# Kernel optimization log

Measured on AMD Instinct MI355X. Metric: run time of the kernel, lower is better.

The kernel has to match this reference:

```python
import jax, jax.numpy as jnp
import numpy as np

BN_EPS = 1e-5

def conv1x1(x, w, b):
    # x: [N,C,T,V], w: [O,C], b: [O]
    return jnp.einsum('nctv,oc->notv', x, w) + b[None, :, None, None]

def conv9(x, w, b):
    # (9,1) temporal conv, padding (4,0). x: [N,C,T,V], w: [O,C,9], b: [O]
    out = jax.lax.conv_general_dilated(
        x, w[:, :, :, None], window_strides=(1, 1), padding=((4, 4), (0, 0)),
        dimension_numbers=('NCHW', 'OIHW', 'NCHW'))
    return out + b[None, :, None, None]

def attn_adj(f1, f2):
    # f1,f2: [N,inter,T,V] -> softmax over rows (axis -2) of [N,V,V]
    N, ic, T, V = f1.shape
    a1 = jnp.transpose(f1, (0, 3, 1, 2)).reshape(N, V, ic * T)  # permute(0,3,1,2).view
    a2 = f2.reshape(N, ic * T, V)
    scores = jnp.einsum('nvk,nkw->nvw', a1, a2) / (ic * T)
    return jax.nn.softmax(scores, axis=-2)


def setup_inputs() -> dict:
    key = jax.random.key(0)
    ks = jax.random.split(key, 16)
    N, C, T, V, S, IC = 16, 256, 64, 25, 3, 64
    s = lambda k, shape, sc=0.05: jax.random.normal(k, shape, dtype=jnp.float32) * sc
    return {
        'x': jax.random.normal(ks[0], (N, C, T, V), dtype=jnp.float32),
        'A': jax.random.uniform(ks[1], (S, V, V), dtype=jnp.float32),
        'PA': s(ks[2], (S, V, V), 1e-3),
        'wa': s(ks[3], (S, IC, C)), 'ba': jnp.zeros((S, IC), jnp.float32),
        'wb': s(ks[4], (S, IC, C)), 'bb': jnp.zeros((S, IC), jnp.float32),
        'wT1': s(ks[5], (S, IC, C, 9)), 'bT1': jnp.zeros((S, IC), jnp.float32),
        'wT2': s(ks[6], (S, IC, C, 9)), 'bT2': jnp.zeros((S, IC), jnp.float32),
        'wST11': s(ks[7], (S, IC, C, 9)), 'bST11': jnp.zeros((S, IC), jnp.float32),
        'wST12': s(ks[8], (S, IC, C, 9)), 'bST12': jnp.zeros((S, IC), jnp.float32),
        'wd': s(ks[9], (S, C, C)), 'bd': jnp.zeros((S, C), jnp.float32),
        'gamma': jnp.ones((C,), jnp.float32), 'beta': jnp.zeros((C,), jnp.float32),
        'bn_mean': jnp.zeros((C,), jnp.float32), 'bn_var': jnp.ones((C,), jnp.float32),
    }


def reference(x, A, PA, wa, ba, wb, bb, wT1, bT1, wT2, bT2,
              wST11, bST11, wST12, bST12, wd, bd, gamma, beta, bn_mean, bn_var):
    N, C, T, V = x.shape
    I = jnp.eye(V, dtype=x.dtype)
    # Chebyshev-like static graph transforms (computed once in __init__ in torch)
    A_ch4s = jax.nn.softmax((8 * A**4 - 4 * A**2 - 4 * A + I) / V, axis=-2)
    A_ch3 = 4 * A**2 - A - 2 * I
    A_all = A_ch3 + A_ch4s + PA  # [3,V,V]

    xf = x.reshape(N, C * T, V)
    y = 0.0
    for i in range(3):
        A1 = attn_adj(conv1x1(x, wa[i], ba[i]), conv1x1(x, wb[i], bb[i]))
        AT = attn_adj(conv9(x, wT1[i], bT1[i]), conv9(x, wT2[i], bT2[i]))
        # ModuleList append quirk: even i -> 1x1 conv (center tap), odd i -> (9,1) conv
        if i % 2 == 0:
            s1 = conv1x1(x, wST11[i, :, :, 4], bST11[i])
            s2 = conv1x1(x, wST12[i, :, :, 4], bST12[i])
        else:
            s1 = conv9(x, wST11[i], bST11[i])
            s2 = conv9(x, wST12[i], bST12[i])
        AST = attn_adj(s1, s2)
        Ai = A_all[i] + A1 + AT + AST  # [N,V,V]
        z = jnp.einsum('nkv,nvw->nkw', xf, Ai).reshape(N, C, T, V)
        y = y + conv1x1(z, wd[i], bd[i])

    yb = (y - bn_mean[None, :, None, None]) * (gamma[None, :, None, None]
         / jnp.sqrt(bn_var[None, :, None, None] + BN_EPS)) + beta[None, :, None, None]
    return jax.nn.relu(yb + x)  # down is identity (in_channels == out_channels)
```

## Files before the change

kernel.cpp:

```cpp
#include <hip/hip_runtime.h>
#include <hip/hip_bf16.h>

#define NN 16
#define CC 256
#define TT 64
#define VV 25
#define ICC 64
#define TV 1600
#define CTV 409600
#define NICTV 1638400

typedef __bf16 v8bf __attribute__((ext_vector_type(8)));
typedef __bf16 v4bf __attribute__((ext_vector_type(4)));
typedef float f32x16 __attribute__((ext_vector_type(16)));

struct ConvPairs {
  const __bf16* wA[5];
  const __bf16* wB[5];
  const float*  bA[5];
  const float*  bB[5];
};

__device__ __forceinline__ void gl_lds16(const __bf16* g, __bf16* l){
  __builtin_amdgcn_global_load_lds(
      (const __attribute__((address_space(1))) unsigned int*)g,
      (__attribute__((address_space(3))) unsigned int*)l, 16, 0, 0);
}

__global__ __launch_bounds__(256) void prep_k(
    const float* __restrict__ x, __bf16* __restrict__ xt,
    const float* __restrict__ wT1, const float* __restrict__ wT2,
    const float* __restrict__ wST11, const float* __restrict__ wST12,
    __bf16* __restrict__ wT1p, __bf16* __restrict__ wT2p,
    __bf16* __restrict__ wS1p, __bf16* __restrict__ wS2p,
    const float* __restrict__ wa, const float* __restrict__ wb,
    __bf16* __restrict__ wabp, __bf16* __restrict__ wScp,
    const float* __restrict__ wd, __bf16* __restrict__ wdb,
    const float* __restrict__ A, const float* __restrict__ PA,
    float* __restrict__ Aall, __bf16* __restrict__ zp){
  __shared__ __align__(16) float smf[64*65];
  __bf16* smb = (__bf16*)smf;
  int b = blockIdx.x;
  int tid = threadIdx.x;
  if (b < 64){
    int t = b >> 3, ch64 = (b >> 1) & 3, o2 = b & 1;
    const float* src; __bf16* dst;
    if (t < 3)      { src = wT1  + (size_t)t*147456;     dst = wT1p + (size_t)t*147456; }
    else if (t < 6) { src = wT2  + (size_t)(t-3)*147456; dst = wT2p + (size_t)(t-3)*147456; }
    else if (t == 6){ src = wST11 + 147456;              dst = wS1p; }
    else            { src = wST12 + 147456;              dst = wS2p; }
    const float* in = src + (size_t)(o2*32)*2304 + ch64*576;
    for (int i = tid; i < 32*576; i += 256){
      int row = i / 576, cc = i % 576;
      smb[i] = (__bf16)in[(size_t)row*2304 + cc];
    }
    __syncthreads();
    for (int i = tid; i < 18432; i += 256){
      int e = i & 7, l = (i >> 3) & 63, ks = (i >> 9) & 1;
      int r10 = i >> 10;
      int tap = r10 % 9, chh = r10 / 9;
      int ol = l & 31, hh = l >> 5;
      int cl = ks*16 + hh*8 + e;
      int c64 = chh*32 + cl;
      int ch8 = ch64*2 + chh;
      dst[(size_t)((((ch8*9 + tap)*2 + ks)*2 + o2)*512) + l*8 + e]
          = smb[ol*576 + c64*9 + tap];
    }
  } else if (b < 74){
    int u = b - 64;
    for (int it = 0; it < 8; ++it){
      int i = tid + it*256;
      int e = i & 7, l = (i >> 3) & 63, o2 = (i >> 9) & 1;
      int ks = (i >> 10) & 1, ch = i >> 11;
      int ol = l & 31, hh = l >> 5;
      int o = o2*32 + ol;
      int c = ch*32 + ks*16 + hh*8 + e;
      __bf16 v;
      if (u < 6){
        const float* w = (u < 3) ? (wa + (size_t)u*16384) : (wb + (size_t)(u-3)*16384);
        v = (__bf16)w[(size_t)o*256 + c];
      } else {
        int i9 = ((u == 6) || (u == 8)) ? 0 : 2;
        const float* w = ((u < 8) ? wST11 : wST12) + (size_t)i9*147456;
        v = (__bf16)w[((size_t)o*256 + c)*9 + 4];
      }
      __bf16* dst = (u < 6) ? (wabp + (size_t)u*16384) : (wScp + (size_t)(u-6)*16384);
      dst[i] = v;
    }
  } else if (b < 842){
    int i = (b-74)*256 + tid;
    if (i < 196608) wdb[i] = (__bf16)wd[i];
  } else if (b == 842){
    int t = tid;
    if (t < 75){
      int s = t / 25, w = t % 25;
      float a[25], m[25];
      float mx = -3.4e38f;
      for (int v = 0; v < 25; ++v){
        float av = A[(s*25 + v)*25 + w];
        a[v] = av;
        float d = (v == w) ? 1.f : 0.f;
        float mm = (8.f*av*av*av*av - 4.f*av*av - 4.f*av + d) * 0.04f;
        m[v] = mm;
        mx = fmaxf(mx, mm);
      }
      float sum = 0.f;
      for (int v = 0; v < 25; ++v){ float e = __expf(m[v]-mx); m[v] = e; sum += e; }
      float inv = 1.f/sum;
      for (int v = 0; v < 25; ++v){
        float av = a[v];
        float d = (v == w) ? 1.f : 0.f;
        Aall[(s*25+v)*25 + w] = m[v]*inv + 4.f*av*av - av - 2.f*d + PA[(s*25+v)*25+w];
      }
    } else if (t >= 128){
      zp[t-128] = (__bf16)0.f;
    }
  } else {
    int idx = b - 843;
    int p0 = (idx % 25)*64, c0 = ((idx/25) & 3)*64, n = idx/100;
    for (int i = tid; i < 4096; i += 256){
      int cc = i >> 6, pp = i & 63;
      smf[cc*65+pp] = x[(size_t)n*CTV + (size_t)(c0+cc)*TV + p0 + pp];
    }
    __syncthreads();
    for (int i = tid; i < 4096; i += 256){
      int pp = i >> 6, cc = i & 63;
      xt[((size_t)n*TV + p0+pp)*256 + c0+cc] = (__bf16)smf[cc*65+pp];
    }
  }
}

template<int NTAPS, int MINW>
__global__ __launch_bounds__(512, MINW) void conv15_k(const __bf16* __restrict__ xt,
    ConvPairs cp, const __bf16* __restrict__ zp, __bf16* __restrict__ fbuf){
  extern __shared__ __bf16 sm[];
  constexpr int HALO  = (NTAPS==9) ? 100 : 0;
  constexpr int NROWS = 256 + 2*HALO;
  constexpr int SLOTS = NROWS*4;
  constexpr int KSTG  = (SLOTS + 511)/512;
  constexpr int NSTEP = NTAPS*2;
  constexpr int AELE  = NTAPS*2*2*512;
  constexpr int ASLT  = 2*AELE/8;
  constexpr int DEP   = (NSTEP >= 3) ? 3 : 2;
  int p0 = blockIdx.x*256;
  int n  = blockIdx.y;
  int pr = blockIdx.z;
  int tid = threadIdx.x;
  int lane = tid & 63;
  int wave = tid >> 6;
  int which = wave >> 2, wq = wave & 3;
  int h = lane >> 5, l31 = lane & 31;
  const __bf16* xtn = xt + (size_t)n*CTV;
  const __bf16* wg0 = cp.wA[pr];
  const __bf16* wg1 = cp.wB[pr];
  __bf16* xb0 = sm;
  __bf16* xb1 = sm + NROWS*32;
  __bf16* Ab  = sm + 2*NROWS*32;

  f32x16 acc[2][2];
  #pragma unroll
  for (int a=0;a<2;++a)
    #pragma unroll
    for (int b=0;b<2;++b)
      #pragma unroll
      for (int r=0;r<16;++r) acc[a][b][r] = 0.f;

  int rowbase = wq*64 + l31;

  auto stageX = [&](__bf16* bn, int ch){
    #pragma unroll
    for (int k=0; k<KSTG; ++k){
      int slot = k*512 + tid;
      if ((SLOTS & 511) && slot >= SLOTS) continue;
      const __bf16* src;
      if (NTAPS == 1){
        int l31s = slot & 31, f = slot >> 5;
        int h_ = f & 1, ks_ = (f >> 1) & 1, pblk = f >> 2;
        int pg = p0 + pblk*32 + l31s;
        src = (pg < 1600) ? (xtn + (size_t)pg*256 + ch*32 + ks_*16 + h_*8)
                          : zp;
      } else {
        int row = slot >> 2, g2 = slot & 3;
        int g = (g2 - (row>>1)) & 3;
        int pg = p0 - HALO + row;
        src = ((unsigned)pg < 1600u) ? (xtn + (size_t)pg*256 + ch*32 + g*8)
                                     : zp;
      }
      gl_lds16(src, bn + (size_t)slot*8);
    }
  };
  auto stageA = [&](int ch){
    #pragma unroll
    for (int k=0; k<(ASLT+511)/512; ++k){
      int slot = k*512 + tid;
      if ((ASLT & 511) && slot >= ASLT) continue;
      int cv = (slot >= AELE/8) ? 1 : 0;
      int off = (slot - cv*(AELE/8))*8;
      const __bf16* src = (cv ? wg1 : wg0) + (size_t)ch*AELE + off;
      gl_lds16(src, Ab + cv*AELE + off);
    }
  };
  const __bf16* aw = Ab + which*AELE + lane*8;
  auto ldA = [&](int s, v8bf* aa){
    int off = s*1024;
    aa[0] = *(const v8bf*)(aw + off);
    aa[1] = *(const v8bf*)(aw + off + 512);
  };
  auto ldB = [&](const __bf16* bc, int s, v8bf* bb){
    int tap = s >> 1, ks = s & 1;
    #pragma unroll
    for (int pq=0; pq<2; ++pq){
      if (NTAPS == 1){
        int frag = ((wq*2 + pq)*2 + ks)*2 + h;
        bb[pq] = *(const v8bf*)(bc + frag*256 + l31*8);
      } else {
        int row = tap*25 + rowbase + pq*32;
        int gs = ((ks*2 + h) + (row>>1)) & 3;
        bb[pq] = *(const v8bf*)(bc + row*32 + gs*8);
      }
    }
  };

  stageA(0);
  stageX(xb0, 0);
  __syncthreads();

  v8bf ar[DEP][2], bR[DEP][2];
  for (int ch=0; ch<8; ++ch){
    const __bf16* bc = (ch & 1) ? xb1 : xb0;
    __bf16*       bn = (ch & 1) ? xb0 : xb1;
    if (ch < 7) stageX(bn, ch+1);
    #pragma unroll
    for (int i=0; i<DEP; ++i){
      if (i < NSTEP){ ldA(i, ar[i]); ldB(bc, i, bR[i]); }
    }
    #pragma unroll
    for (int s=0; s<NSTEP; ++s){
      int c = s % DEP;
      v8bf A0 = ar[c][0], A1 = ar[c][1];
      v8bf B0 = bR[c][0], B1 = bR[c][1];
      if (s+DEP < NSTEP){
        ldB(bc, s+DEP, bR[c]);
        ldA(s+DEP, ar[c]);
      }
      __builtin_amdgcn_s_setprio(1);
      acc[0][0] = __builtin_amdgcn_mfma_f32_32x32x16_bf16(A0, B0, acc[0][0], 0,0,0);
      acc[1][0] = __builtin_amdgcn_mfma_f32_32x32x16_bf16(A1, B0, acc[1][0], 0,0,0);
      acc[0][1] = __builtin_amdgcn_mfma_f32_32x32x16_bf16(A0, B1, acc[0][1], 0,0,0);
      acc[1][1] = __builtin_amdgcn_mfma_f32_32x32x16_bf16(A1, B1, acc[1][1], 0,0,0);
      __builtin_amdgcn_s_setprio(0);
    }
    __syncthreads();
    if (ch < 7) stageA(ch+1);
    __syncthreads();
  }

  const float* bias = which ? cp.bB[pr] : cp.bA[pr];
  __bf16* outb = fbuf + (size_t)(pr*2 + which)*NICTV + (size_t)n*TV*64;
  #pragma unroll
  for (int pq=0; pq<2; ++pq){
    int p = p0 + wq*64 + pq*32 + l31;
    if (p >= 1600) continue;
    __bf16* orow = outb + (size_t)p*64;
    #pragma unroll
    for (int of=0; of<2; ++of){
      #pragma unroll
      for (int g=0; g<4; ++g){
        int og = of*32 + 8*g + 4*h;
        v4bf pk;
        #pragma unroll
        for (int j=0;j<4;++j) pk[j] = (__bf16)(acc[of][pq][4*g+j] + bias[og+j]);
        *(v4bf*)(orow + og) = pk;
      }
    }
  }
}

__global__ __launch_bounds__(256, 2) void ugemm6_k(const __bf16* __restrict__ xt,
    const __bf16* __restrict__ wdb, __bf16* __restrict__ ubuf){
  __shared__ __bf16 sm[64*256];
  int p0 = blockIdx.x*64;
  int n  = blockIdx.y;
  int tid = threadIdx.x;
  int lane = tid & 63;
  int os = tid >> 6;
  int h = lane >> 5, l31 = lane & 31;
  const __bf16* xtn = xt + (size_t)n*CTV;

  for (int s2 = tid; s2 < 64*32; s2 += 256){
    int row = s2 >> 5, g = s2 & 31;
    uint4 val = *(const uint4*)(xtn + (size_t)(p0+row)*256 + g*8);
    int gs = (g + row) & 31;
    *(uint4*)(sm + row*256 + gs*8) = val;
  }
  __syncthreads();

  auto ldB = [&](int ks, v8bf* bb){
    #pragma unroll
    for (int pq=0; pq<2; ++pq){
      int row = pq*32 + l31;
      int gs = ((ks*2 + h) + row) & 31;
      bb[pq] = *(const v8bf*)(sm + row*256 + gs*8);
    }
  };

  for (int br=0; br<3; ++br){
    const __bf16* wl = wdb + ((size_t)br*256 + os*64 + l31)*256 + h*8;
    auto ldA = [&](int ks, v8bf& A0, v8bf& A1){
      A0 = *(const v8bf*)(wl + ks*16);
      A1 = *(const v8bf*)(wl + (size_t)32*256 + ks*16);
    };
    f32x16 acc[2][2];
    #pragma unroll
    for (int a=0;a<2;++a)
      #pragma unroll
      for (int b=0;b<2;++b)
        #pragma unroll
        for (int r=0;r<16;++r) acc[a][b][r] = 0.f;

    v8bf a0[4], a1[4];
    ldA(0, a0[0], a1[0]);
    ldA(1, a0[1], a1[1]);
    ldA(2, a0[2], a1[2]);
    ldA(3, a0[3], a1[3]);
    v8bf bR[2][2];
    ldB(0, bR[0]);
    ldB(1, bR[1]);
    #pragma unroll
    for (int ks=0; ks<16; ++ks){
      int c2 = ks & 1, cur = ks & 3;
      v8bf B0 = bR[c2][0], B1 = bR[c2][1];
      v8bf A0 = a0[cur], A1 = a1[cur];
      if (ks+2 < 16) ldB(ks+2, bR[c2]);
      if (ks+4 < 16) ldA(ks+4, a0[cur], a1[cur]);
      acc[0][0] = __builtin_amdgcn_mfma_f32_32x32x16_bf16(A0, B0, acc[0][0], 0,0,0);
      acc[1][0] = __builtin_amdgcn_mfma_f32_32x32x16_bf16(A1, B0, acc[1][0], 0,0,0);
      acc[0][1] = __builtin_amdgcn_mfma_f32_32x32x16_bf16(A0, B1, acc[0][1], 0,0,0);
      acc[1][1] = __builtin_amdgcn_mfma_f32_32x32x16_bf16(A1, B1, acc[1][1], 0,0,0);
    }

    #pragma unroll
    for (int pq=0; pq<2; ++pq){
      int p = p0 + pq*32 + l31;
      __bf16* out = ubuf + ((size_t)(br*NN + n)*TV + p)*256;
      #pragma unroll
      for (int oq=0; oq<2; ++oq){
        #pragma unroll
        for (int g=0; g<4; ++g){
          int og = os*64 + oq*32 + 8*g + 4*h;
          v4bf pk;
          #pragma unroll
          for (int j=0;j<4;++j) pk[j] = (__bf16)acc[oq][pq][4*g+j];
          *(v4bf*)(out + og) = pk;
        }
      }
    }
  }
}

__global__ __launch_bounds__(256) void scores_m_k(const __bf16* __restrict__ fbuf,
                                                  float* __restrict__ part, int pairbase){
  int n = blockIdx.y, pr = blockIdx.z;
  int tid = threadIdx.x;
  int lane = tid & 63;
  int wave = tid >> 6;
  int chunk = blockIdx.x*4 + wave;
  int h = lane >> 5, l31 = lane & 31;
  const __bf16* f1 = fbuf + (size_t)(pr*2)*NICTV   + (size_t)n*TV*64;
  const __bf16* f2 = fbuf + (size_t)(pr*2+1)*NICTV + (size_t)n*TV*64;
  int t0 = chunk*4;

  f32x16 acc;
  #pragma unroll
  for (int r=0;r<16;++r) acc[r] = 0.f;

  auto off = [&](int s)->size_t{
    int t = t0 + (s>>2), og = s&3;
    return ((size_t)(t*25 + l31))*64 + og*16 + h*8;
  };
  v8bf A[4], B[4];
  #pragma unroll
  for (int i=0; i<4; ++i){
    size_t o = off(i);
    A[i] = *(const v8bf*)(f1+o); B[i] = *(const v8bf*)(f2+o);
  }
  #pragma unroll
  for (int s=0; s<16; ++s){
    int cur = s & 3;
    v8bf Ac = A[cur], Bc = B[cur];
    if (s+4 < 16){
      size_t o2 = off(s+4);
      A[cur] = *(const v8bf*)(f1+o2);
      B[cur] = *(const v8bf*)(f2+o2);
    }
    acc = __builtin_amdgcn_mfma_f32_32x32x16_bf16(Ac, Bc, acc, 0,0,0);
  }

  size_t tile = (((size_t)(pairbase+pr)*NN + n)*16 + chunk);
  float* pt = part + tile*1024;
  #pragma unroll
  for (int r=0; r<16; ++r){
    int row = (r&3) + 8*(r>>2) + 4*h;
    pt[row*32 + l31] = acc[r];
  }
}

__global__ __launch_bounds__(64) void reduce_all_k(const float* __restrict__ part,
    const float* __restrict__ Aall, float* __restrict__ Ai3){
  const int pairbr[9] = {0,1,2,0,2, 0,1,2,1};
  int n = blockIdx.x, w = blockIdx.y;
  int lane = threadIdx.x;
  float accbr[3] = {0.f, 0.f, 0.f};
  for (int pr=0; pr<9; ++pr){
    float s = 0.f;
    if (lane < 25){
      const float* pp = part + (((size_t)pr*NN + n)*16)*1024 + lane*32 + w;
      #pragma unroll
      for (int ch=0; ch<16; ++ch) s += pp[(size_t)ch*1024];
    }
    s *= (1.f/4096.f);
    float mval = (lane<25) ? s : -3.4e38f;
    #pragma unroll
    for (int d=32; d>0; d>>=1) mval = fmaxf(mval, __shfl_xor(mval, d));
    float e = (lane<25) ? __expf(s - mval) : 0.f;
    float sum = e;
    #pragma unroll
    for (int d=32; d>0; d>>=1) sum += __shfl_xor(sum, d);
    accbr[pairbr[pr]] += e / sum;
  }
  if (lane < 25){
    #pragma unroll
    for (int br=0; br<3; ++br)
      Ai3[((size_t)br*NN + n)*625 + lane*25 + w] =
        Aall[br*625 + lane*25 + w] + accbr[br];
  }
}

__global__ __launch_bounds__(256) void yep_k(const float* __restrict__ x,
    const float* __restrict__ Ai3, const __bf16* __restrict__ ubuf,
    const float* __restrict__ bd, const float* __restrict__ gamma,
    const float* __restrict__ beta, const float* __restrict__ bnm,
    const float* __restrict__ bnv, float* __restrict__ out){
  __shared__ float ais[3][25*28];
  int t = blockIdx.x, n = blockIdx.y, o = threadIdx.x;
  for (int l=o; l<2100; l+=256){
    int br = l/700, r = l%700;
    int v = r/28, w = r%28;
    ais[br][v*28+w] = (w<25) ? Ai3[((size_t)br*NN + n)*625 + v*25 + w] : 0.f;
  }
  __syncthreads();
  float y[28];
  #pragma unroll
  for (int w=0;w<28;++w) y[w]=0.f;
  for (int br=0; br<3; ++br){
    const __bf16* up = ubuf + ((size_t)(br*NN + n)*TV + t*25)*256 + o;
    float uv[25];
    #pragma unroll
    for (int v=0;v<25;++v) uv[v] = (float)up[(size_t)v*256];
    const float* ab = ais[br];
    for (int v=0; v<25; ++v){
      float u = uv[v];
      #pragma unroll
      for (int j=0; j<7; ++j){
        float4 a4 = *(const float4*)(ab + v*28 + 4*j);
        y[4*j+0] = fmaf(u, a4.x, y[4*j+0]);
        y[4*j+1] = fmaf(u, a4.y, y[4*j+1]);
        y[4*j+2] = fmaf(u, a4.z, y[4*j+2]);
        y[4*j+3] = fmaf(u, a4.w, y[4*j+3]);
      }
    }
  }
  float bsum = bd[o] + bd[256+o] + bd[512+o];
  float sc = gamma[o] * rsqrtf(bnv[o] + 1e-5f);
  float m  = bnm[o], be = beta[o];
  const float* xr = x + (size_t)n*CTV + (size_t)o*TV + t*25;
  float* orow = out + (size_t)n*CTV + (size_t)o*TV + t*25;
  #pragma unroll
  for (int w=0; w<25; ++w)
    orow[w] = fmaxf((y[w] + bsum - m)*sc + be + xr[w], 0.f);
}

extern "C" void kernel_launch(void* const* d_in, const int* in_sizes, int n_in,
                              void* d_out, int out_size, void* d_ws, size_t ws_size,
                              hipStream_t stream) {
  const float* x     = (const float*)d_in[0];
  const float* A     = (const float*)d_in[1];
  const float* PA    = (const float*)d_in[2];
  const float* wa    = (const float*)d_in[3];
  const float* ba    = (const float*)d_in[4];
  const float* wb    = (const float*)d_in[5];
  const float* bb    = (const float*)d_in[6];
  const float* wT1   = (const float*)d_in[7];
  const float* bT1   = (const float*)d_in[8];
  const float* wT2   = (const float*)d_in[9];
  const float* bT2   = (const float*)d_in[10];
  const float* wST11 = (const float*)d_in[11];
  const float* bST11 = (const float*)d_in[12];
  const float* wST12 = (const float*)d_in[13];
  const float* bST12 = (const float*)d_in[14];
  const float* wd    = (const float*)d_in[15];
  const float* bd    = (const float*)d_in[16];
  const float* gamma = (const float*)d_in[17];
  const float* beta  = (const float*)d_in[18];
  const float* bnm   = (const float*)d_in[19];
  const float* bnv   = (const float*)d_in[20];

  char* W = (char*)d_ws;
  float*  Aall = (float*)W;  W += 8192;
  __bf16* zp   = (__bf16*)W; W += 256;
  float*  Ai3  = (float*)W;  W += 122880;
  __bf16* wabp = (__bf16*)W; W += 196608;
  __bf16* wScp = (__bf16*)W; W += 131072;
  __bf16* wT1p = (__bf16*)W; W += 884736;
  __bf16* wT2p = (__bf16*)W; W += 884736;
  __bf16* wS1p = (__bf16*)W; W += 294912;
  __bf16* wS2p = (__bf16*)W; W += 294912;
  __bf16* wdb  = (__bf16*)W; W += 393216;
  __bf16* xt   = (__bf16*)W; W += 13107200;
  char* R = W;               W += 39321600;
  float*  part = (float*)W;  W += 9437184;
  __bf16* fbuf = (__bf16*)R;
  __bf16* ubuf = (__bf16*)R;

  prep_k<<<2443, 256, 0, stream>>>(x, xt, wT1, wT2, wST11, wST12,
                                   wT1p, wT2p, wS1p, wS2p,
                                   wa, wb, wabp, wScp, wd, wdb, A, PA, Aall, zp);

  {
    ConvPairs cp;
    for (int i=0;i<3;++i){
      cp.wA[i] = wabp + (size_t)i*16384;      cp.wB[i] = wabp + (size_t)(3+i)*16384;
      cp.bA[i] = ba + i*64;                   cp.bB[i] = bb + i*64;
    }
    int evens[2] = {0, 2};
    for (int j=0;j<2;++j){
      int i = evens[j];
      cp.wA[3+j] = wScp + (size_t)j*16384;    cp.wB[3+j] = wScp + (size_t)(2+j)*16384;
      cp.bA[3+j] = bST11 + i*64;              cp.bB[3+j] = bST12 + i*64;
    }
    conv15_k<1,4><<<dim3(7,16,5), 512, 40960, stream>>>(xt, cp, zp, fbuf);
    scores_m_k<<<dim3(4,16,5), 256, 0, stream>>>(fbuf, part, 0);
  }

  {
    ConvPairs cp;
    for (int i=0;i<3;++i){
      cp.wA[i] = wT1p + (size_t)i*147456;  cp.wB[i] = wT2p + (size_t)i*147456;
      cp.bA[i] = bT1 + i*64;               cp.bB[i] = bT2 + i*64;
    }
    cp.wA[3] = wS1p;  cp.wB[3] = wS2p;
    cp.bA[3] = bST11 + 64;  cp.bB[3] = bST12 + 64;
    cp.wA[4] = cp.wA[3]; cp.wB[4] = cp.wB[3]; cp.bA[4] = cp.bA[3]; cp.bB[4] = cp.bB[3];
    conv15_k<9,2><<<dim3(7,16,4), 512, 132096, stream>>>(xt, cp, zp, fbuf);
    scores_m_k<<<dim3(4,16,4), 256, 0, stream>>>(fbuf, part, 5);
  }

  ugemm6_k<<<dim3(25,16), 256, 0, stream>>>(xt, wdb, ubuf);
  reduce_all_k<<<dim3(16,25), 64, 0, stream>>>(part, Aall, Ai3);
  yep_k<<<dim3(64,16), 256, 0, stream>>>(x, Ai3, ubuf, bd, gamma, beta, bnm, bnv,
                                         (float*)d_out);
}
```

Before: 328.4 us.

## Pre-reduce score partials in LDS, restructure softmax finalize, coalesce epilogue via LDS

The scores kernel now sums its four waves' 32x32 partial tiles in shared memory before writing, so the partial buffer holds 4 tiles per (pair,n) instead of 16. The finalize kernel is regrouped per (n, branch) with one thread per column that computes the softmax serially over 25 rows, replacing the shuffle-based per-column launch. The yep epilogue stages x and out through shared memory so global reads and writes are contiguous across threads instead of strided by TV. The changes add syncs and shared-memory use, and the finalize kernel runs only 48 small blocks.

New measurement: 354.8 us. +8.0%, slower.

```diff
diff --git a/kernel.cpp b/kernel.cpp
--- a/kernel.cpp
+++ b/kernel.cpp
@@ -358,13 +358,14 @@
   }
 }
 
-__global__ __launch_bounds__(256) void scores_m_k(const __bf16* __restrict__ fbuf,
-                                                  float* __restrict__ part, int pairbase){
-  int n = blockIdx.y, pr = blockIdx.z;
+__global__ __launch_bounds__(256) void scores_m2_k(const __bf16* __restrict__ fbuf,
+                                                   float* __restrict__ part, int pairbase){
+  __shared__ float smp[4][1024];
+  int bx = blockIdx.x, n = blockIdx.y, pr = blockIdx.z;
   int tid = threadIdx.x;
   int lane = tid & 63;
   int wave = tid >> 6;
-  int chunk = blockIdx.x*4 + wave;
+  int chunk = bx*4 + wave;
   int h = lane >> 5, l31 = lane & 31;
   const __bf16* f1 = fbuf + (size_t)(pr*2)*NICTV   + (size_t)n*TV*64;
   const __bf16* f2 = fbuf + (size_t)(pr*2+1)*NICTV + (size_t)n*TV*64;
@@ -396,43 +397,53 @@
     acc = __builtin_amdgcn_mfma_f32_32x32x16_bf16(Ac, Bc, acc, 0,0,0);
   }
 
-  size_t tile = (((size_t)(pairbase+pr)*NN + n)*16 + chunk);
-  float* pt = part + tile*1024;
   #pragma unroll
   for (int r=0; r<16; ++r){
     int row = (r&3) + 8*(r>>2) + 4*h;
-    pt[row*32 + l31] = acc[r];
-  }
-}
-
-__global__ __launch_bounds__(64) void reduce_all_k(const float* __restrict__ part,
+    smp[wave][row*32 + l31] = acc[r];
+  }
+  __syncthreads();
+  for (int j = tid; j < 1024; j += 256){
+    float s = smp[0][j] + smp[1][j] + smp[2][j] + smp[3][j];
+    part[(((size_t)(pairbase+pr)*NN + n)*4 + bx)*1024 + j] = s;
+  }
+}
+
+__global__ __launch_bounds__(64) void finalize_k(const float* __restrict__ part,
     const float* __restrict__ Aall, float* __restrict__ Ai3){
-  const int pairbr[9] = {0,1,2,0,2, 0,1,2,1};
-  int n = blockIdx.x, w = blockIdx.y;
-  int lane = threadIdx.x;
-  float accbr[3] = {0.f, 0.f, 0.f};
-  for (int pr=0; pr<9; ++pr){
-    float s = 0.f;
-    if (lane < 25){
-      const float* pp = part + (((size_t)pr*NN + n)*16)*1024 + lane*32 + w;
-      #pragma unroll
-      for (int ch=0; ch<16; ++ch) s += pp[(size_t)ch*1024];
-    }
-    s *= (1.f/4096.f);
-    float mval = (lane<25) ? s : -3.4e38f;
-    #pragma unroll
-    for (int d=32; d>0; d>>=1) mval = fmaxf(mval, __shfl_xor(mval, d));
-    float e = (lane<25) ? __expf(s - mval) : 0.f;
-    float sum = e;
-    #pragma unroll
-    for (int d=32; d>0; d>>=1) sum += __shfl_xor(sum, d);
-    accbr[pairbr[pr]] += e / sum;
-  }
-  if (lane < 25){
-    #pragma unroll
-    for (int br=0; br<3; ++br)
-      Ai3[((size_t)br*NN + n)*625 + lane*25 + w] =
-        Aall[br*625 + lane*25 + w] + accbr[br];
+  int n = blockIdx.x, br = blockIdx.y;
+  int w = threadIdx.x;
+  const int prs0[3] = {0,3,5}, prs1[3] = {1,6,8}, prs2[3] = {2,4,7};
+  const int* prs = (br==0) ? prs0 : (br==1) ? prs1 : prs2;
+  float accv[25];
+  #pragma unroll
+  for (int v=0;v<25;++v) accv[v] = 0.f;
+  for (int k=0;k<3;++k){
+    int pr = prs[k];
+    const float* pb = part + ((size_t)pr*NN + n)*4096;
+    float sv[25];
+    float mx = -3.4e38f;
+    #pragma unroll
+    for (int v=0;v<25;++v){
+      float s = 0.f;
+      if (w < 25)
+        s = pb[v*32+w] + pb[1024+v*32+w] + pb[2048+v*32+w] + pb[3072+v*32+w];
+      s *= (1.f/4096.f);
+      sv[v] = s;
+      mx = fmaxf(mx, s);
+    }
+    float sum = 0.f;
+    #pragma unroll
+    for (int v=0;v<25;++v){ float e = __expf(sv[v]-mx); sv[v] = e; sum += e; }
+    float inv = 1.f/sum;
+    #pragma unroll
+    for (int v=0;v<25;++v) accv[v] += sv[v]*inv;
+  }
+  if (w < 25){
+    #pragma unroll
+    for (int v=0;v<25;++v)
+      Ai3[((size_t)br*NN + n)*625 + v*25 + w] =
+        Aall[br*625 + v*25 + w] + accv[v];
   }
 }
 
@@ -442,11 +453,16 @@
     const float* __restrict__ beta, const float* __restrict__ bnm,
     const float* __restrict__ bnv, float* __restrict__ out){
   __shared__ float ais[3][25*28];
+  __shared__ float xs[6400];
   int t = blockIdx.x, n = blockIdx.y, o = threadIdx.x;
   for (int l=o; l<2100; l+=256){
     int br = l/700, r = l%700;
     int v = r/28, w = r%28;
     ais[br][v*28+w] = (w<25) ? Ai3[((size_t)br*NN + n)*625 + v*25 + w] : 0.f;
+  }
+  for (int li=o; li<6400; li+=256){
+    int oo = li/25, ww = li%25;
+    xs[li] = x[(size_t)n*CTV + (size_t)oo*TV + t*25 + ww];
   }
   __syncthreads();
   float y[28];
@@ -473,11 +489,14 @@
   float bsum = bd[o] + bd[256+o] + bd[512+o];
   float sc = gamma[o] * rsqrtf(bnv[o] + 1e-5f);
   float m  = bnm[o], be = beta[o];
-  const float* xr = x + (size_t)n*CTV + (size_t)o*TV + t*25;
-  float* orow = out + (size_t)n*CTV + (size_t)o*TV + t*25;
   #pragma unroll
   for (int w=0; w<25; ++w)
-    orow[w] = fmaxf((y[w] + bsum - m)*sc + be + xr[w], 0.f);
+    xs[o*25+w] = fmaxf((y[w] + bsum - m)*sc + be + xs[o*25+w], 0.f);
+  __syncthreads();
+  for (int li=o; li<6400; li+=256){
+    int oo = li/25, ww = li%25;
+    out[(size_t)n*CTV + (size_t)oo*TV + t*25 + ww] = xs[li];
+  }
 }
 
 extern "C" void kernel_launch(void* const* d_in, const int* in_sizes, int n_in,
@@ -518,7 +537,7 @@
   __bf16* wdb  = (__bf16*)W; W += 393216;
   __bf16* xt   = (__bf16*)W; W += 13107200;
   char* R = W;               W += 39321600;
-  float*  part = (float*)W;  W += 9437184;
+  float*  part = (float*)W;  W += 2359296;
   __bf16* fbuf = (__bf16*)R;
   __bf16* ubuf = (__bf16*)R;
 
@@ -539,7 +558,7 @@
       cp.bA[3+j] = bST11 + i*64;              cp.bB[3+j] = bST12 + i*64;
     }
     conv15_k<1,4><<<dim3(7,16,5), 512, 40960, stream>>>(xt, cp, zp, fbuf);
-    scores_m_k<<<dim3(4,16,5), 256, 0, stream>>>(fbuf, part, 0);
+    scores_m2_k<<<dim3(4,16,5), 256, 0, stream>>>(fbuf, part, 0);
   }
 
   {
@@ -552,11 +571,11 @@
     cp.bA[3] = bST11 + 64;  cp.bB[3] = bST12 + 64;
     cp.wA[4] = cp.wA[3]; cp.wB[4] = cp.wB[3]; cp.bA[4] = cp.bA[3]; cp.bB[4] = cp.bB[3];
     conv15_k<9,2><<<dim3(7,16,4), 512, 132096, stream>>>(xt, cp, zp, fbuf);
-    scores_m_k<<<dim3(4,16,4), 256, 0, stream>>>(fbuf, part, 5);
+    scores_m2_k<<<dim3(4,16,4), 256, 0, stream>>>(fbuf, part, 5);
   }
 
   ugemm6_k<<<dim3(25,16), 256, 0, stream>>>(xt, wdb, ubuf);
-  reduce_all_k<<<dim3(16,25), 64, 0, stream>>>(part, Aall, Ai3);
+  finalize_k<<<dim3(16,3), 64, 0, stream>>>(part, Aall, Ai3);
   yep_k<<<dim3(64,16), 256, 0, stream>>>(x, Ai3, ubuf, bd, gamma, beta, bnm, bnv,
                                          (float*)d_out);
 }
```
